# Performance work log

Hardware: AMD Instinct MI355X
Metric: run time of the kernel (lower is better)

## Reference

```python
import jax, jax.numpy as jnp
import numpy as np

B, T, D = 32, 200, 256
H, DH = 4, 32
INNER = H * DH  # 128
L, FF, NI = 8, 1024, 100000
NB = 64  # gap/recency buckets


def _ln(x, g, b, eps=1e-5):
    m = x.mean(-1, keepdims=True)
    v = jnp.mean((x - m) ** 2, -1, keepdims=True)
    return (x - m) / jnp.sqrt(v + eps) * g + b


def _gelu(x):
    return jax.nn.gelu(x, approximate=False)


def _dwconv_causal(x, w, b):
    # x: [B,T,C], w: [C,k] depthwise kernel, causal left-pad (k-1)
    k = w.shape[1]
    xp = jnp.pad(x, ((0, 0), (k - 1, 0), (0, 0))).transpose(0, 2, 1)  # [B,C,T+k-1]
    out = jax.lax.conv_general_dilated(
        xp, w[:, None, :], (1,), 'VALID',
        dimension_numbers=('NCH', 'OIH', 'NCH'), feature_group_count=w.shape[0])
    return out.transpose(0, 2, 1) + b


def _causal_linear_attention(q, k, v, m4):
    q = (jax.nn.elu(q) + 1.0) * m4
    k = (jax.nn.elu(k) + 1.0) * m4
    v = v * m4
    kv = jnp.einsum('bthd,bthe->bthde', k, v)          # [B,T,H,DH,DH]
    kv_prefix = jnp.cumsum(kv, axis=1)
    k_prefix = jnp.cumsum(k, axis=1)
    num = jnp.einsum('bthd,bthde->bthe', q, kv_prefix)
    den = jnp.sum(q * k_prefix, -1, keepdims=True)
    return num / (den + 1e-6) * m4


def _forward(item_emb, pos_emb, gap_emb, rec_emb, tf_w1, tf_b1, tf_w2, tf_b2,
             in_g, in_b, l_ln1g, l_ln1b, l_win, l_bin, l_wc, l_bc, l_tw, l_tb,
             l_pw, l_pb, l_wmix, l_bmix, l_ln2g, l_ln2b, l_wf1, l_bf1, l_wf2, l_bf2,
             fn_g, fn_b, pg_w, pg_b, uh_w1, uh_b1, uh_lng, uh_lnb, uh_w2, uh_b2,
             item_bias, ids, ts, lens):
    Bb, Tt = ids.shape
    pos = jnp.arange(Tt)
    mask = pos[None, :] >= (Tt - lens)[:, None]  # right-aligned valid mask [B,T]
    prev_ts = jnp.roll(ts, 1, axis=1)
    prev_mask = jnp.roll(mask, 1, axis=1).at[:, 0].set(False)
    zero = jnp.zeros_like(ts)
    gap_vals = jnp.where(mask & prev_mask, jnp.maximum(ts - prev_ts, 0), zero)
    latest = ts[:, -1:]
    rec_vals = jnp.where(mask, jnp.maximum(latest - ts, 0), zero)

    def buck(v, n):
        vf = jnp.maximum(v.astype(jnp.float32), 0.0)
        return jnp.clip(jnp.floor(jnp.log2(vf + 1.0)), 0, n - 1).astype(jnp.int32)

    gb = buck(gap_vals, NB)
    rb = buck(rec_vals, NB)
    rec_raw = jnp.maximum(latest - ts, 0).astype(jnp.float32)
    tf = jnp.stack([jnp.log1p(gb.astype(jnp.float32)), jnp.log1p(rec_raw)], -1)  # [B,T,2]
    dense_time = _gelu(tf @ tf_w1 + tf_b1) @ tf_w2 + tf_b2

    x = item_emb[ids] + pos_emb[None] + gap_emb[gb] + rec_emb[rb] + dense_time
    mf = mask[..., None].astype(x.dtype)
    m4 = mask[..., None, None].astype(x.dtype)
    x = _ln(x, in_g, in_b) * mf

    for i in range(L):
        res = x
        nrm = _ln(x, l_ln1g[i], l_ln1b[i])
        proj = nrm @ l_win[i] + l_bin[i]  # [B,T,D+3*INNER]
        gate = proj[..., :D]
        q = proj[..., D:D + INNER].reshape(Bb, Tt, H, DH)
        k = proj[..., D + INNER:D + 2 * INNER].reshape(Bb, Tt, H, DH)
        v = proj[..., D + 2 * INNER:].reshape(Bb, Tt, H, DH)
        content = _causal_linear_attention(q, k, v, m4).reshape(Bb, Tt, INNER) @ l_wc[i] + l_bc[i]
        temporal = _dwconv_causal(nrm, l_tw[i], l_tb[i])
        positional = _dwconv_causal(nrm, l_pw[i], l_pb[i])
        mixed = jnp.concatenate([content, temporal, positional], -1) @ l_wmix[i] + l_bmix[i]
        x = (res + jax.nn.sigmoid(gate) * mixed) * mf
        h = _ln(x, l_ln2g[i], l_ln2b[i])
        ffn = _gelu(h @ l_wf1[i] + l_bf1[i]) @ l_wf2[i] + l_bf2[i]
        x = (x + ffn) * mf

    x = _ln(x, fn_g, fn_b) * mf
    denom = jnp.maximum(lens, 1)[:, None].astype(x.dtype)
    mean_pooled = (x * mf).sum(1) / denom
    ps = (x @ pg_w + pg_b)[..., 0]
    ps = jnp.where(mask, ps, -1e9)
    pw = jax.nn.softmax(ps, axis=1)[..., None]
    attn_pooled = (pw * x).sum(1)
    last = x[:, -1, :]
    u = jnp.concatenate([last, mean_pooled, attn_pooled], -1)
    u = _gelu(u @ uh_w1 + uh_b1)
    u = _ln(u, uh_lng, uh_lnb)
    u = u @ uh_w2 + uh_b2
    u = u / jnp.maximum(jnp.linalg.norm(u, axis=-1, keepdims=True), 1e-12)
    ie = item_emb[1:]
    ie = ie / jnp.maximum(jnp.linalg.norm(ie, axis=-1, keepdims=True), 1e-12)
    return u @ ie.T + item_bias[1:]


def setup_inputs() -> dict:
    key = jax.random.key(0)
    it = iter(jax.random.split(key, 64))
    def nk():
        return next(it)
    def w(*s):
        return jax.random.normal(nk(), s, jnp.float32) * 0.02
    inp = dict(
        history_ids=jax.random.randint(nk(), (B, T), 0, NI),
        history_timestamps=jnp.sort(jax.random.randint(nk(), (B, T), 0, 1000000), axis=1),
        history_lengths=jax.random.randint(nk(), (B,), 1, T + 1),
        item_emb=w(NI + 1, D).at[0].set(0.0),
        pos_emb=w(T, D), gap_emb=w(NB, D), rec_emb=w(NB, D),
        tf_w1=w(2, D), tf_b1=jnp.zeros((D,)), tf_w2=w(D, D), tf_b2=jnp.zeros((D,)),
        in_g=jnp.ones((D,)), in_b=jnp.zeros((D,)),
        l_ln1g=jnp.ones((L, D)), l_ln1b=jnp.zeros((L, D)),
        l_win=w(L, D, D + 3 * INNER), l_bin=jnp.zeros((L, D + 3 * INNER)),
        l_wc=w(L, INNER, D), l_bc=jnp.zeros((L, D)),
        l_tw=w(L, D, 3), l_tb=jnp.zeros((L, D)),
        l_pw=w(L, D, 5), l_pb=jnp.zeros((L, D)),
        l_wmix=w(L, 3 * D, D), l_bmix=jnp.zeros((L, D)),
        l_ln2g=jnp.ones((L, D)), l_ln2b=jnp.zeros((L, D)),
        l_wf1=w(L, D, FF), l_bf1=jnp.zeros((L, FF)),
        l_wf2=w(L, FF, D), l_bf2=jnp.zeros((L, D)),
        fn_g=jnp.ones((D,)), fn_b=jnp.zeros((D,)),
        pg_w=w(D, 1), pg_b=jnp.zeros((1,)),
        uh_w1=w(3 * D, 1024), uh_b1=jnp.zeros((1024,)),
        uh_lng=jnp.ones((1024,)), uh_lnb=jnp.zeros((1024,)),
        uh_w2=w(1024, D), uh_b2=jnp.zeros((D,)),
        item_bias=jnp.zeros((NI + 1,)),
    )
    return inp


def reference(history_ids, history_timestamps, history_lengths, item_emb, pos_emb,
              gap_emb, rec_emb, tf_w1, tf_b1, tf_w2, tf_b2, in_g, in_b, l_ln1g,
              l_ln1b, l_win, l_bin, l_wc, l_bc, l_tw, l_tb, l_pw, l_pb, l_wmix,
              l_bmix, l_ln2g, l_ln2b, l_wf1, l_bf1, l_wf2, l_bf2, fn_g, fn_b,
              pg_w, pg_b, uh_w1, uh_b1, uh_lng, uh_lnb, uh_w2, uh_b2, item_bias):
    return _forward(item_emb, pos_emb, gap_emb, rec_emb, tf_w1, tf_b1, tf_w2, tf_b2,
                    in_g, in_b, l_ln1g, l_ln1b, l_win, l_bin, l_wc, l_bc, l_tw, l_tb,
                    l_pw, l_pb, l_wmix, l_bmix, l_ln2g, l_ln2b, l_wf1, l_bf1, l_wf2,
                    l_bf2, fn_g, fn_b, pg_w, pg_b, uh_w1, uh_b1, uh_lng, uh_lnb,
                    uh_w2, uh_b2, item_bias, history_ids, history_timestamps,
                    history_lengths)
```

## Files before the change

kernel.cpp:

```cpp
#include <hip/hip_runtime.h>
#include <math.h>

#define B_ 32
#define T_ 200
#define D_ 256
#define H_ 4
#define DH_ 32
#define INNER_ 128
#define L_ 8
#define FF_ 1024
#define NI_ 100000
#define NB_ 64
#define CH_ 25

typedef __attribute__((ext_vector_type(8))) short short8;
typedef __attribute__((ext_vector_type(8))) unsigned short ushort8;
typedef __attribute__((ext_vector_type(4))) unsigned short ushort4v;
typedef __attribute__((ext_vector_type(4))) float floatx4;

__device__ __forceinline__ float gelu_f(float x){
  return 0.5f*x*(1.0f+erff(x*0.70710678118654752f));
}
__device__ __forceinline__ float wsum(float v){
  #pragma unroll
// ... 155 lines not shown
      int m0 = bm + wm + 16*i + kg*4;
      #pragma unroll
      for (int r=0;r<4;r++){
        int m = m0 + r;
        if (m < M){
          float v = acc[i][j][r] + bv;
          if (mode == 1) v = gelu_f(v);
          float* cp = &C[(size_t)m*ldC + n];
          if (mode == 2) v += *cp;
          *cp = v;
        }
      }
    }
  }
}

template<int K, int NJ>
__global__ __launch_bounds__(256) void k_gemm16(
    const unsigned short* __restrict__ A, const unsigned short* __restrict__ Wt,
    const float* __restrict__ bias, void* __restrict__ Cv,
    int ldA, int ldW, int ldC, int mode)
{
  int tid = threadIdx.x;
  int wave = tid >> 6, lane = tid & 63;
  int frow = lane & 15, kg = lane >> 4;
  int bm = blockIdx.y * 32;
  int bn = blockIdx.x * (64*NJ) + wave * (16*NJ);

  const unsigned short* a0 = A + (size_t)(bm + frow)*ldA + kg*8;
  const unsigned short* a1 = a0 + (size_t)16*ldA;
  const unsigned short* b0 = Wt + (size_t)(bn + frow)*ldW + kg*8;

  floatx4 acc[2][NJ];
  #pragma unroll
  for (int i=0;i<2;i++)
    #pragma unroll
    for (int j=0;j<NJ;j++) acc[i][j] = (floatx4){0.f,0.f,0.f,0.f};

  #pragma unroll
  for (int k0=0; k0<K; k0+=32){
    short8 af0 = *(const short8*)(a0 + k0);
    short8 af1 = *(const short8*)(a1 + k0);
    #pragma unroll
    for (int j=0;j<NJ;j++){
      short8 bf = *(const short8*)(b0 + (size_t)j*16*ldW + k0);
      acc[0][j] = __builtin_amdgcn_mfma_f32_16x16x32_bf16(af0, bf, acc[0][j], 0, 0, 0);
      acc[1][j] = __builtin_amdgcn_mfma_f32_16x16x32_bf16(af1, bf, acc[1][j], 0, 0, 0);
    }
  }

  float* Cf = (float*)Cv;
  unsigned short* Ch = (unsigned short*)Cv;
  #pragma unroll
  for (int j=0;j<NJ;j++){
    int n = bn + 16*j + frow;
    float bv = bias[n];
    #pragma unroll
    for (int i=0;i<2;i++){
      int m0 = bm + 16*i + kg*4;
      #pragma unroll
      for (int r=0;r<4;r++){
        float v = acc[i][j][r] + bv;
        size_t off = (size_t)(m0+r)*ldC + n;
        if (mode == 1)      Cf[off] = gelu_f(v);
        else if (mode == 2) Cf[off] += v;
        else if (mode == 4) Ch[off] = f2bf(gelu_f(v));
        else                Cf[off] = v;
      }
    }
  }
}

__global__ __launch_bounds__(256) void k_proj(
  const unsigned short* __restrict__ A, const unsigned short* __restrict__ Wt,
  const float* __restrict__ bias, const int* __restrict__ lens,
  unsigned short* __restrict__ gateb, unsigned short* __restrict__ phiQ,
  unsigned short* __restrict__ phiK, unsigned short* __restrict__ vB,
  const float* __restrict__ tw, const float* __restrict__ tb,
  const float* __restrict__ pw, const float* __restrict__ pb,
  unsigned short* __restrict__ cat)
{
  int bid = blockIdx.x;
  int tid = threadIdx.x;
  if (bid < 400){
    int wave = tid >> 6, lane = tid & 63;
    int frow = lane & 15, kg = lane >> 4;
    int bx = bid & 1, by = bid >> 1;
    int bm = by * 32;
    int wn = bx*320 + wave*80;
    const unsigned short* a0 = A + (size_t)(bm + frow)*256 + kg*8;
    const unsigned short* a1 = a0 + (size_t)16*256;
    const unsigned short* b0 = Wt + (size_t)(wn + frow)*256 + kg*8;
    floatx4 acc[2][5];
    #pragma unroll
    for (int i=0;i<2;i++)
      #pragma unroll
      for (int j=0;j<5;j++) acc[i][j] = (floatx4){0.f,0.f,0.f,0.f};
    #pragma unroll
    for (int k0=0; k0<256; k0+=32){
      short8 af0 = *(const short8*)(a0 + k0);
      short8 af1 = *(const short8*)(a1 + k0);
      #pragma unroll
      for (int j=0;j<5;j++){
        short8 bf = *(const short8*)(b0 + (size_t)j*16*256 + k0);
        acc[0][j] = __builtin_amdgcn_mfma_f32_16x16x32_bf16(af0, bf, acc[0][j], 0, 0, 0);
        acc[1][j] = __builtin_amdgcn_mfma_f32_16x16x32_bf16(af1, bf, acc[1][j], 0, 0, 0);
      }
    }
    #pragma unroll
    for (int i=0;i<2;i++){
      #pragma unroll
      for (int r=0;r<4;r++){
        int row = bm + 16*i + kg*4 + r;
        int t = row % T_, b = row / T_;
        float m = (t >= T_ - lens[b]) ? 1.f : 0.f;
        #pragma unroll
        for (int j=0;j<5;j++){
          int n = wn + 16*j + frow;
          float v = acc[i][j][r] + bias[n];
          if (n < 256){
            gateb[(size_t)row*256 + n] = f2bf(v);
          } else if (n < 384){
            int bh = b*4 + ((n-256)>>5), dd = n & 31;
            phiQ[(size_t)bh*6400 + t*32 + dd] = f2bf((v > 0.f ? v + 1.f : __expf(v))*m);
          } else if (n < 512){
            int bh = b*4 + ((n-384)>>5), dd = n & 31;
            phiK[(size_t)bh*6400 + t*32 + dd] = f2bf((v > 0.f ? v + 1.f : __expf(v))*m);
          } else {
            int bh = b*4 + ((n-512)>>5), dd = n & 31;
            vB[(size_t)bh*6400 + t*32 + dd] = f2bf(v*m);
          }
        }
      }
    }
  } else {
    int bid2 = bid - 400;
    int d = tid;
    int bt0 = bid2*4;
    float xs8[8];
    #pragma unroll
    for (int w=0;w<8;w++){
      int wr = bt0 - 4 + w;
      xs8[w] = (wr >= 0) ? bf2f(A[(size_t)wr*256 + d]) : 0.f;
    }
    #pragma unroll
    for (int rr=0;rr<4;rr++){
      int bt = bt0 + rr, t = bt % T_;
      float ot = tb[d], op = pb[d];
      #pragma unroll
      for (int j=0;j<5;j++){
        int tt = t - 4 + j;
        float xv = (tt >= 0) ? xs8[rr+j] : 0.f;
        op += pw[d*5+j]*xv;
        if (j >= 2) ot += tw[d*3 + (j-2)]*xv;
      }
      cat[(size_t)bt*640 + 128 + d] = f2bf(ot);
      cat[(size_t)bt*640 + 384 + d] = f2bf(op);
    }
  }
}

template<int K, int MODE>
__global__ __launch_bounds__(256) void k_gemmln(
    const unsigned short* __restrict__ A, const unsigned short* __restrict__ Wt,
    const float* __restrict__ bias, float* __restrict__ xbuf,
    const unsigned short* __restrict__ gateb, const int* __restrict__ lens,
    const float* __restrict__ g, const float* __restrict__ bb,
    unsigned short* __restrict__ nrm, int maskLN)
{
  __shared__ float rs[16][4];
  __shared__ float rq[16][4];
  int tid = threadIdx.x;
  int wave = tid >> 6, lane = tid & 63;
  int frow = lane & 15, kg = lane >> 4;
  int bm = blockIdx.x * 16;
  int wn = wave * 64;

  const unsigned short* a0 = A + (size_t)(bm + frow)*K + kg*8;
  const unsigned short* b0 = Wt + (size_t)(wn + frow)*K + kg*8;

  floatx4 acc[4];
  #pragma unroll
  for (int j=0;j<4;j++) acc[j] = (floatx4){0.f,0.f,0.f,0.f};

  #pragma unroll
  for (int k0=0; k0<K; k0+=32){
    short8 af0 = *(const short8*)(a0 + k0);
    #pragma unroll
    for (int j=0;j<4;j++){
      short8 bf = *(const short8*)(b0 + (size_t)16*j*K + k0);
      acc[j] = __builtin_amdgcn_mfma_f32_16x16x32_bf16(af0, bf, acc[j], 0, 0, 0);
    }
  }

  float xn[4][4];
  float rowm[4];
  #pragma unroll
  for (int r=0;r<4;r++){
    int row = bm + kg*4 + r;
    int t = row % T_, b = row / T_;
    float m = (t >= T_ - lens[b]) ? 1.f : 0.f;
    rowm[r] = m;
    #pragma unroll
    for (int j=0;j<4;j++){
      int n = wn + 16*j + frow;
      float v = acc[j][r] + bias[n];
      float xv = xbuf[(size_t)row*256 + n];
      float xnv;
      if (MODE == 0){
        float gv = bf2f(gateb[(size_t)row*256 + n]);
        xnv = (xv + v/(1.f+__expf(-gv)))*m;
      } else {
        xnv = (xv + v)*m;
      }
      xn[j][r] = xnv;
      xbuf[(size_t)row*256 + n] = xnv;
    }
  }
  float mu[4];
  #pragma unroll
  for (int r=0;r<4;r++){
    float s = xn[0][r]+xn[1][r]+xn[2][r]+xn[3][r];
    s += __shfl_xor(s,1,64); s += __shfl_xor(s,2,64);
    s += __shfl_xor(s,4,64); s += __shfl_xor(s,8,64);
    if (frow == 0) rs[kg*4 + r][wave] = s;
  }
  __syncthreads();
  #pragma unroll
  for (int r=0;r<4;r++){
    int rl = kg*4 + r;
    mu[r] = (rs[rl][0]+rs[rl][1]+rs[rl][2]+rs[rl][3]) * (1.f/256.f);
  }
  float rstd[4];
  #pragma unroll
  for (int r=0;r<4;r++){
    float m0 = mu[r];
    float s = 0.f;
    #pragma unroll
    for (int j=0;j<4;j++){ float d = xn[j][r]-m0; s += d*d; }
    s += __shfl_xor(s,1,64); s += __shfl_xor(s,2,64);
    s += __shfl_xor(s,4,64); s += __shfl_xor(s,8,64);
    if (frow == 0) rq[kg*4 + r][wave] = s;
  }
  __syncthreads();
  #pragma unroll
  for (int r=0;r<4;r++){
    int rl = kg*4 + r;
    float q = rq[rl][0]+rq[rl][1]+rq[rl][2]+rq[rl][3];
    rstd[r] = rsqrtf(q*(1.f/256.f) + 1e-5f);
  }
  #pragma unroll
  for (int r=0;r<4;r++){
    int row = bm + kg*4 + r;
    float ml = maskLN ? rowm[r] : 1.f;
    #pragma unroll
    for (int j=0;j<4;j++){
      int n = wn + 16*j + frow;
      float h = (xn[j][r]-mu[r])*rstd[r]*g[n] + bb[n];
      nrm[(size_t)row*256 + n] = f2bf(h*ml);
    }
  }
}

__global__ __launch_bounds__(256) void k_embed(
  const int* __restrict__ ids, const int* __restrict__ ts, const int* __restrict__ lens,
  const float* __restrict__ item_emb, const float* __restrict__ pos_emb,
  const float* __restrict__ gap_emb, const float* __restrict__ rec_emb,
  const float* __restrict__ tf_w1, const float* __restrict__ tf_b1,
  float* __restrict__ xbuf, unsigned short* __restrict__ tfh)
{
  int bt = blockIdx.x;
  int b = bt / T_, t = bt % T_;
  int d = threadIdx.x;
  int len = lens[b];
  int tcur = ts[b*T_+t];
  int tlast = ts[b*T_+T_-1];
  bool mask  = t >= T_ - len;
  bool pmask = (t >= 1) && ((t-1) >= T_ - len);
  int gap = 0;
  if (mask && pmask){ int pv = ts[b*T_+t-1]; gap = max(tcur - pv, 0); }
  int rec = mask ? max(tlast - tcur, 0) : 0;
  int gb = min(max((int)floorf(log2f((float)gap + 1.0f)), 0), NB_-1);
  int rb = min(max((int)floorf(log2f((float)rec + 1.0f)), 0), NB_-1);
  float rec_raw = (float)max(tlast - tcur, 0);
  float tf0 = log1pf((float)gb);
  float tf1 = log1pf(rec_raw);
  float hid = gelu_f(tf0*tf_w1[d] + tf1*tf_w1[D_+d] + tf_b1[d]);
  tfh[(size_t)bt*D_ + d] = f2bf(hid);
  int id = ids[b*T_+t];
  xbuf[(size_t)bt*D_ + d] = item_emb[(size_t)id*D_ + d] + pos_emb[t*D_ + d]
                          + gap_emb[gb*D_ + d] + rec_emb[rb*D_ + d];
}

template<int NC>
__global__ __launch_bounds__(256) void k_ln(
  const float* __restrict__ in, void* __restrict__ out,
  const float* __restrict__ g, const float* __restrict__ bb,
  int rows, const int* __restrict__ lens, int applyMask, int outBf)
{
  int wid = threadIdx.x >> 6, lane = threadIdx.x & 63;
  int r = blockIdx.x*4 + wid;
  if (r >= rows) return;
  const int D = NC*256;
  const float4* rp = (const float4*)(in + (size_t)r*D);
  float4 v[NC];
  float s = 0.f;
  #pragma unroll
  for (int c=0;c<NC;c++){ v[c] = rp[c*64 + lane]; s += v[c].x+v[c].y+v[c].z+v[c].w; }
  s = wsum(s);
  float mean = s / (float)D;
  float q = 0.f;
  #pragma unroll
  for (int c=0;c<NC;c++){
    float a=v[c].x-mean, b2=v[c].y-mean, c2=v[c].z-mean, d2=v[c].w-mean;
    q += a*a + b2*b2 + c2*c2 + d2*d2;
  }
  q = wsum(q);
  float rstd = rsqrtf(q/(float)D + 1e-5f);
  float m = 1.f;
  if (applyMask){ int t = r % T_; int b = r / T_; m = (t >= T_ - lens[b]) ? 1.f : 0.f; }
  #pragma unroll
  for (int c=0;c<NC;c++){
    float4 gg  = ((const float4*)g )[c*64+lane];
    float4 bv  = ((const float4*)bb)[c*64+lane];
    float4 o;
    o.x = ((v[c].x-mean)*rstd*gg.x + bv.x)*m;
    o.y = ((v[c].y-mean)*rstd*gg.y + bv.y)*m;
    o.z = ((v[c].z-mean)*rstd*gg.z + bv.z)*m;
    o.w = ((v[c].w-mean)*rstd*gg.w + bv.w)*m;
    if (outBf){
      ushort4v ob; ob.x=f2bf(o.x); ob.y=f2bf(o.y); ob.z=f2bf(o.z); ob.w=f2bf(o.w);
      ((ushort4v*)((unsigned short*)out + (size_t)r*D))[c*64+lane] = ob;
    } else {
      ((float4*)((float*)out + (size_t)r*D))[c*64+lane] = o;
    }
  }
}

__global__ __launch_bounds__(256) void k_lnln(
  float* __restrict__ x, const int* __restrict__ lens,
  const float* __restrict__ g1, const float* __restrict__ b1,
  const float* __restrict__ g2, const float* __restrict__ b2,
  unsigned short* __restrict__ nrm)
{
  int wid = threadIdx.x >> 6, lane = threadIdx.x & 63;
  int r = blockIdx.x*4 + wid;
  int t = r % T_, b = r / T_;
  float m = (t >= T_ - lens[b]) ? 1.f : 0.f;
  float4 v = ((const float4*)(x + (size_t)r*256))[lane];
  float s = wsum(v.x+v.y+v.z+v.w);
  float mean = s/256.f;
  float a=v.x-mean, b2v=v.y-mean, c2=v.z-mean, d2=v.w-mean;
  float q = wsum(a*a+b2v*b2v+c2*c2+d2*d2);
  float rstd = rsqrtf(q/256.f + 1e-5f);
  float4 gg = ((const float4*)g1)[lane];
  float4 bv = ((const float4*)b1)[lane];
  float4 xn;
  xn.x = (a*rstd*gg.x + bv.x)*m;
  xn.y = (b2v*rstd*gg.y + bv.y)*m;
  xn.z = (c2*rstd*gg.z + bv.z)*m;
  xn.w = (d2*rstd*gg.w + bv.w)*m;
  ((float4*)(x + (size_t)r*256))[lane] = xn;
  float s2 = wsum(xn.x+xn.y+xn.z+xn.w);
  float mean2 = s2/256.f;
  float a2=xn.x-mean2, b22=xn.y-mean2, c22=xn.z-mean2, d22=xn.w-mean2;
  float q2 = wsum(a2*a2+b22*b22+c22*c22+d22*d22);
  float rstd2 = rsqrtf(q2/256.f + 1e-5f);
  float4 gg2 = ((const float4*)g2)[lane];
  float4 bv2 = ((const float4*)b2)[lane];
  ushort4v o;
  o.x = f2bf(a2*rstd2*gg2.x + bv2.x);
  o.y = f2bf(b22*rstd2*gg2.y + bv2.y);
  o.z = f2bf(c22*rstd2*gg2.z + bv2.z);
  o.w = f2bf(d22*rstd2*gg2.w + bv2.w);
  ((ushort4v*)(nrm + (size_t)r*256))[lane] = o;
}

__global__ __launch_bounds__(128) void k_attn_sums(
  const unsigned short* __restrict__ phiK, const unsigned short* __restrict__ vB,
  float* __restrict__ Ssum)
{
  int blk = blockIdx.x;
  int bh = blk >> 3, c = blk & 7;
  int tid = threadIdx.x; int e = tid & 31, q = tid >> 5;
  __shared__ float sk[CH_*32], sv[CH_*32];
  size_t base = (size_t)bh*6400 + (size_t)c*CH_*32;
  for (int idx = tid; idx < CH_*32; idx += 128){
    sk[idx] = bf2f(phiK[base + idx]);
    sv[idx] = bf2f(vB[base + idx]);
  }
  __syncthreads();
  float acc[8];
  #pragma unroll
  for (int j=0;j<8;j++) acc[j]=0.f;
  for (int tl=0; tl<CH_; tl++){
    const float4* k4 = (const float4*)(sk + tl*32 + q*8);
    float vf = sv[tl*32 + e];
    float4 ka = k4[0], kb = k4[1];
    acc[0]+=ka.x*vf; acc[1]+=ka.y*vf; acc[2]+=ka.z*vf; acc[3]+=ka.w*vf;
    acc[4]+=kb.x*vf; acc[5]+=kb.y*vf; acc[6]+=kb.z*vf; acc[7]+=kb.w*vf;
  }
  float* dst = Ssum + ((size_t)bh*8 + c)*1056;
  #pragma unroll
  for (int j=0;j<8;j++) dst[(q*8+j)*32 + e] = acc[j];
  if (q == 0){
    float s = 0.f;
    for (int tl=0; tl<CH_; tl++) s += sk[tl*32 + e];
    dst[1024 + e] = s;
  }
}

__global__ __launch_bounds__(256) void k_attn_out(
  const unsigned short* __restrict__ phiQ, const unsigned short* __restrict__ phiK,
  const unsigned short* __restrict__ vB, const int* __restrict__ lens,
  const float* __restrict__ Ssum, unsigned short* __restrict__ cat)
{
  int blk = blockIdx.x;
  int bh = blk >> 3, c = blk & 7;
  int b = bh >> 2, h = bh & 3;
  int tid = threadIdx.x; int e = tid & 31, qg = tid >> 5;
  int tstart = T_ - lens[b];
  __shared__ float sq[CH_*32], sk[CH_*32], sv[CH_*32];
  __shared__ float P[1056];
  __shared__ float A[CH_][CH_+1];
  __shared__ float sden[CH_];
  int t0 = c*CH_;
  const float* basep = Ssum + (size_t)bh*8*1056;
  for (int idx = tid; idx < 1056; idx += 256){
    float s = 0.f;
    for (int cp=0; cp<c; cp++) s += basep[(size_t)cp*1056 + idx];
    P[idx] = s;
  }
  size_t base = (size_t)bh*6400 + (size_t)c*CH_*32;
  for (int idx = tid; idx < CH_*32; idx += 256){
    sq[idx] = bf2f(phiQ[base + idx]);
    sk[idx] = bf2f(phiK[base + idx]);
    sv[idx] = bf2f(vB[base + idx]);
  }
  __syncthreads();
  for (int idx = tid; idx < CH_*CH_; idx += 256){
    int t = idx / CH_, tp = idx - t*CH_;
    float s = 0.f;
    if (tp <= t){
      const float4* q4 = (const float4*)(sq + t*32);
      const float4* k4 = (const float4*)(sk + tp*32);
      #pragma unroll
      for (int jj=0;jj<8;jj++){
        float4 qq = q4[jj], kk = k4[jj];
        s += qq.x*kk.x + qq.y*kk.y + qq.z*kk.z + qq.w*kk.w;
      }
    }
    A[t][tp] = s;
  }
  __syncthreads();
  if (tid < CH_){
    int t = tid;
    float s = 0.f;
    for (int tp=0; tp<=t; tp++) s += A[t][tp];
    const float* qf = sq + t*32;
    #pragma unroll
    for (int d=0; d<32; d++) s += qf[d]*P[1024+d];
    sden[t] = s;
  }
  __syncthreads();
  int tlo = (qg*CH_) >> 3, thi = ((qg+1)*CH_) >> 3;
  for (int t = tlo; t < thi; t++){
    float num = 0.f;
    for (int tp=0; tp<=t; tp++) num += A[t][tp]*sv[tp*32+e];
    const float* qf = sq + t*32;
    #pragma unroll
    for (int d=0; d<32; d++) num += qf[d]*P[d*32+e];
    int tg = t0 + t;
    float m = (tg >= tstart) ? 1.f : 0.f;
    cat[(size_t)(b*T_+tg)*640 + h*32 + e] = f2bf(num/(sden[t]+1e-6f)*m);
  }
}

__global__ __launch_bounds__(256) void k_pool(
  const unsigned short* __restrict__ x, const int* __restrict__ lens,
  const float* __restrict__ pg_w, const float* __restrict__ pg_b,
  float* __restrict__ u0)
{
  int b = blockIdx.x;
  int tid = threadIdx.x, wid = tid>>6, lane = tid&63;
  __shared__ float sps[T_];
  __shared__ float spw[T_];
  int len = lens[b]; int tstart = T_ - len;
  const float4* pw4 = (const float4*)pg_w;
  float4 wv = pw4[lane];
  for (int t = wid; t < T_; t += 4){
    ushort4v xv = ((const ushort4v*)(x + (size_t)(b*T_+t)*D_))[lane];
    float dot = bf2f(xv.x)*wv.x + bf2f(xv.y)*wv.y + bf2f(xv.z)*wv.z + bf2f(xv.w)*wv.w;
    dot = wsum(dot);
    if (lane==0) sps[t] = (t >= tstart) ? dot + pg_b[0] : -1e9f;
  }
  __syncthreads();
  float mx = -1e30f;
  for (int t=0;t<T_;t++) mx = fmaxf(mx, sps[t]);
  float sum = 0.f;
  for (int t=0;t<T_;t++) sum += __expf(sps[t]-mx);
  float inv = 1.f/sum;
  if (tid < T_) spw[tid] = __expf(sps[tid]-mx)*inv;
  __syncthreads();
  int d = tid;
  float macc=0.f, aacc=0.f;
  for (int t=0;t<T_;t++){
    float v = bf2f(x[(size_t)(b*T_+t)*D_ + d]);
    macc += v;
    aacc += spw[t]*v;
  }
  u0[b*768 + d]       = bf2f(x[(size_t)(b*T_+T_-1)*D_ + d]);
  u0[b*768 + 256 + d] = macc / (float)max(len,1);
  u0[b*768 + 512 + d] = aacc;
}

__global__ __launch_bounds__(64) void k_norm(float* __restrict__ u, unsigned short* __restrict__ ub)
{
  int b = blockIdx.x; int lane = threadIdx.x;
  float4* r = (float4*)(u + b*256);
  float4 v = r[lane];
  float ss = v.x*v.x + v.y*v.y + v.z*v.z + v.w*v.w;
  ss = wsum(ss);
  float sc = 1.f/fmaxf(sqrtf(ss), 1e-12f);
  v.x*=sc; v.y*=sc; v.z*=sc; v.w*=sc;
  r[lane]=v;
  ub[b*256 + lane*4 + 0] = f2bf(v.x);
  ub[b*256 + lane*4 + 1] = f2bf(v.y);
  ub[b*256 + lane*4 + 2] = f2bf(v.z);
  ub[b*256 + lane*4 + 3] = f2bf(v.w);
}

__global__ __launch_bounds__(256) void k_score2(
  const float* __restrict__ item_emb, const unsigned short* __restrict__ ub,
  const float* __restrict__ item_bias, float* __restrict__ out)
{
  int tid = threadIdx.x;
  int wave = tid >> 6, lane = tid & 63;
  int frow = lane & 15, kg = lane >> 4;
  int n0 = blockIdx.x * 128 + wave * 32;

  int g0 = n0 + frow, g1 = n0 + 16 + frow;
  bool ok0 = g0 < NI_, ok1 = g1 < NI_;
  const float* ip0 = item_emb + (size_t)(g0+1)*256 + kg*8;
  const float* ip1 = item_emb + (size_t)(g1+1)*256 + kg*8;
  const unsigned short* up0 = ub + frow*256 + kg*8;
  const unsigned short* up1 = up0 + 16*256;

  floatx4 acc[2][2];
  #pragma unroll
  for (int i=0;i<2;i++)
    #pragma unroll
    for (int j=0;j<2;j++) acc[i][j] = (floatx4){0.f,0.f,0.f,0.f};
  float ss0 = 0.f, ss1 = 0.f;

  #pragma unroll
  for (int k0=0; k0<256; k0+=32){
    float4 a0, a1, c0, c1;
    if (ok0){ a0 = *(const float4*)(ip0 + k0); a1 = *(const float4*)(ip0 + k0 + 4); }
// ... 34 lines not shown
    }
    #pragma unroll
    for (int j=0;j<2;j++){
      int row = 16*j + frow;
      float4 o;
      o.x = acc[i][j][0]*sc[0] + bv[0];
      o.y = acc[i][j][1]*sc[1] + bv[1];
      o.z = acc[i][j][2]*sc[2] + bv[2];
      o.w = acc[i][j][3]*sc[3] + bv[3];
      *(float4*)&out[(size_t)row*NI_ + nb] = o;
    }
  }
}

extern "C" void kernel_launch(void* const* d_in, const int* in_sizes, int n_in,
                              void* d_out, int out_size, void* d_ws, size_t ws_size,
                              hipStream_t stream)
{
  const int* ids  = (const int*)d_in[0];
  const int* ts   = (const int*)d_in[1];
  const int* lens = (const int*)d_in[2];
  const float* item_emb = (const float*)d_in[3];
  const float* pos_emb  = (const float*)d_in[4];
  const float* gap_emb  = (const float*)d_in[5];
  const float* rec_emb  = (const float*)d_in[6];
  const float* tf_w1 = (const float*)d_in[7];
  const float* tf_b1 = (const float*)d_in[8];
  const float* tf_w2 = (const float*)d_in[9];
  const float* tf_b2 = (const float*)d_in[10];
  const float* in_g  = (const float*)d_in[11];
  const float* in_b  = (const float*)d_in[12];
  const float* l_ln1g = (const float*)d_in[13];
  const float* l_ln1b = (const float*)d_in[14];
  const float* l_win  = (const float*)d_in[15];
  const float* l_bin  = (const float*)d_in[16];
  const float* l_wc   = (const float*)d_in[17];
  const float* l_bc   = (const float*)d_in[18];
  const float* l_tw   = (const float*)d_in[19];
  const float* l_tb   = (const float*)d_in[20];
  const float* l_pw   = (const float*)d_in[21];
  const float* l_pb   = (const float*)d_in[22];
  const float* l_wmix = (const float*)d_in[23];
  const float* l_bmix = (const float*)d_in[24];
  const float* l_ln2g = (const float*)d_in[25];
  const float* l_ln2b = (const float*)d_in[26];
  const float* l_wf1  = (const float*)d_in[27];
  const float* l_bf1  = (const float*)d_in[28];
  const float* l_wf2  = (const float*)d_in[29];
  const float* l_bf2  = (const float*)d_in[30];
  const float* fn_g = (const float*)d_in[31];
  const float* fn_b = (const float*)d_in[32];
  const float* pg_w = (const float*)d_in[33];
  const float* pg_b = (const float*)d_in[34];
  const float* uh_w1 = (const float*)d_in[35];
  const float* uh_b1 = (const float*)d_in[36];
  const float* uh_lng = (const float*)d_in[37];
  const float* uh_lnb = (const float*)d_in[38];
  const float* uh_w2 = (const float*)d_in[39];
  const float* uh_b2 = (const float*)d_in[40];
  const float* item_bias = (const float*)d_in[41];
  float* out = (float*)d_out;

  const int MT = B_*T_;
  float* ws   = (float*)d_ws;
  float* xbuf = ws;
  float* tmp  = xbuf + (size_t)MT*D_;
  float* proj = tmp  + (size_t)MT*D_;
  float* cat  = proj + (size_t)MT*640;
  float* mid  = cat  + (size_t)MT*640;
  float* u0   = mid  + (size_t)MT*FF_;
  float* u1   = u0 + 32*768;
  float* u2   = u1 + 32*1024;
  float* WcombF = u2 + 32*256;
  float* bmixP  = WcombF + 262144;
  float* Ssum   = bmixP + 2048;
  unsigned short* WtPerm = (unsigned short*)(Ssum + 1081344);
  unsigned short* WtMixT = WtPerm + 5505024;
  unsigned short* WtBig  = WtMixT + 1572864;
  unsigned short* WtH    = WtBig  + 1310720;
  unsigned short* u2b    = WtH    + 1114112;

  unsigned short* tmpb = (unsigned short*)tmp;
  unsigned short* catb = (unsigned short*)cat;
  unsigned short* midb = (unsigned short*)(mid + (size_t)MT*D_);
  unsigned short* gateb = (unsigned short*)proj;
  unsigned short* phiQ  = gateb + 1638400;
  unsigned short* phiK  = phiQ + 819200;
  unsigned short* vBuf  = phiK + 819200;

  k_cvtAll<<<8008, 256, 0, stream>>>(l_win, l_wmix, l_wf1, l_wf2, tf_w2, uh_w1, uh_w2,
                                     WtPerm, WtMixT, WtH, l_bc, l_bmix, bmixP);
  k_gemm_bf<64><<<dim3(4,1,8), 256, 0, stream>>>(l_wc, WtMixT, nullptr, WcombF,
                                                 128, 256, 256, 256, 768, 256, 0,
                                                 (size_t)128*256, (size_t)196608, (size_t)32768, 0);
  k_asm<<<64, 256, 0, stream>>>(WcombF, WtMixT, WtBig);

  k_embed<<<MT, 256, 0, stream>>>(ids, ts, lens, item_emb, pos_emb, gap_emb, rec_emb,
                                  tf_w1, tf_b1, xbuf, tmpb);
  k_gemm16<256,2><<<dim3(2,200), 256, 0, stream>>>(tmpb, WtH, tf_b2, xbuf, 256, 256, 256, 2);
  k_lnln<<<MT/4, 256, 0, stream>>>(xbuf, lens, in_g, in_b, l_ln1g, l_ln1b, tmpb);

  for (int i=0;i<L_;i++){
    const unsigned short* WL = WtPerm + (size_t)i*688128;
    k_proj<<<2000, 256, 0, stream>>>(tmpb, WL, l_bin+i*640, lens,
                                     gateb, phiQ, phiK, vBuf,
                                     l_tw+i*768, l_tb+i*256, l_pw+i*1280, l_pb+i*256, catb);
    k_attn_sums<<<B_*H_*8, 128, 0, stream>>>(phiK, vBuf, Ssum);
    k_attn_out<<<B_*H_*8, 256, 0, stream>>>(phiQ, phiK, vBuf, lens, Ssum, catb);
    k_gemmln<640,0><<<400, 256, 0, stream>>>(catb, WtBig+(size_t)i*163840, bmixP+i*256,
                                             xbuf, gateb, lens,
                                             l_ln2g+i*256, l_ln2b+i*256, tmpb, 0);
    k_gemm16<256,4><<<dim3(4,200), 256, 0, stream>>>(tmpb, WL+163840, l_bf1+i*FF_, midb,
                                                     256, 256, FF_, 4);
    bool last = (i == L_-1);
    k_gemmln<1024,1><<<400, 256, 0, stream>>>(midb, WL+425984, l_bf2+i*256,
                                              xbuf, nullptr, lens,
                                              last ? fn_g : l_ln1g+(i+1)*256,
                                              last ? fn_b : l_ln1b+(i+1)*256,
                                              tmpb, last ? 1 : 0);
  }

  k_pool<<<B_, 256, 0, stream>>>(tmpb, lens, pg_w, pg_b, u0);
  k_gemm_bf<128><<<dim3(8,1), 256, 0, stream>>>(u0, WtH+65536, uh_b1, u1,
                                                32, 1024, 768, 768, 768, 1024, 1, 0,0,0,0);
  k_ln<4><<<8, 256, 0, stream>>>(u1, u1, uh_lng, uh_lnb, 32, lens, 0, 0);
  k_gemm_bf<64><<<dim3(4,1), 256, 0, stream>>>(u1, WtH+851968, uh_b2, u2,
                                               32, 256, 1024, 1024, 1024, 256, 0, 0,0,0,0);
  k_norm<<<B_, 64, 0, stream>>>(u2, u2b);

  k_score2<<<(NI_+127)/128, 256, 0, stream>>>(item_emb, u2b, item_bias, out);
}
```

Before: 1.687 ms.

## Fuse attention passes and the mix+LN+FFN+LN chain into single kernels

Merges the two attention kernels into one that recomputes prefix KV sums from earlier chunks in shared memory instead of going through a global Ssum buffer. Fuses the mix GEMM, gated residual, LN2, both FFN GEMMs with GELU, residual and the next LN into one per-16-row kernel that keeps the hidden activations in LDS, removing the mid buffer round trip and two launches per layer. It also halves the k_proj row tile to double its block count. In exchange the attention does redundant prefix work for later chunks, and the fused MLP has only 400 blocks with heavy LDS use and reloads the FFN weights per block.

```diff
diff --git a/kernel.cpp b/kernel.cpp
--- a/kernel.cpp
+++ b/kernel.cpp
@@ -261,59 +261,51 @@
 {
   int bid = blockIdx.x;
   int tid = threadIdx.x;
-  if (bid < 400){
+  if (bid < 800){
     int wave = tid >> 6, lane = tid & 63;
     int frow = lane & 15, kg = lane >> 4;
     int bx = bid & 1, by = bid >> 1;
-    int bm = by * 32;
+    int bm = by * 16;
     int wn = bx*320 + wave*80;
     const unsigned short* a0 = A + (size_t)(bm + frow)*256 + kg*8;
-    const unsigned short* a1 = a0 + (size_t)16*256;
     const unsigned short* b0 = Wt + (size_t)(wn + frow)*256 + kg*8;
-    floatx4 acc[2][5];
-    #pragma unroll
-    for (int i=0;i<2;i++)
-      #pragma unroll
-      for (int j=0;j<5;j++) acc[i][j] = (floatx4){0.f,0.f,0.f,0.f};
+    floatx4 acc[5];
+    #pragma unroll
+    for (int j=0;j<5;j++) acc[j] = (floatx4){0.f,0.f,0.f,0.f};
     #pragma unroll
     for (int k0=0; k0<256; k0+=32){
       short8 af0 = *(const short8*)(a0 + k0);
-      short8 af1 = *(const short8*)(a1 + k0);
       #pragma unroll
       for (int j=0;j<5;j++){
         short8 bf = *(const short8*)(b0 + (size_t)j*16*256 + k0);
-        acc[0][j] = __builtin_amdgcn_mfma_f32_16x16x32_bf16(af0, bf, acc[0][j], 0, 0, 0);
-        acc[1][j] = __builtin_amdgcn_mfma_f32_16x16x32_bf16(af1, bf, acc[1][j], 0, 0, 0);
+        acc[j] = __builtin_amdgcn_mfma_f32_16x16x32_bf16(af0, bf, acc[j], 0, 0, 0);
       }
     }
     #pragma unroll
-    for (int i=0;i<2;i++){
+    for (int r=0;r<4;r++){
+      int row = bm + kg*4 + r;
+      int t = row % T_, b = row / T_;
+      float m = (t >= T_ - lens[b]) ? 1.f : 0.f;
       #pragma unroll
-      for (int r=0;r<4;r++){
-        int row = bm + 16*i + kg*4 + r;
-        int t = row % T_, b = row / T_;
-        float m = (t >= T_ - lens[b]) ? 1.f : 0.f;
-        #pragma unroll
-        for (int j=0;j<5;j++){
-          int n = wn + 16*j + frow;
-          float v = acc[i][j][r] + bias[n];
-          if (n < 256){
-            gateb[(size_t)row*256 + n] = f2bf(v);
-          } else if (n < 384){
-            int bh = b*4 + ((n-256)>>5), dd = n & 31;
-            phiQ[(size_t)bh*6400 + t*32 + dd] = f2bf((v > 0.f ? v + 1.f : __expf(v))*m);
-          } else if (n < 512){
-            int bh = b*4 + ((n-384)>>5), dd = n & 31;
-            phiK[(size_t)bh*6400 + t*32 + dd] = f2bf((v > 0.f ? v + 1.f : __expf(v))*m);
-          } else {
-            int bh = b*4 + ((n-512)>>5), dd = n & 31;
-            vB[(size_t)bh*6400 + t*32 + dd] = f2bf(v*m);
-          }
+      for (int j=0;j<5;j++){
+        int n = wn + 16*j + frow;
+        float v = acc[j][r] + bias[n];
+        if (n < 256){
+          gateb[(size_t)row*256 + n] = f2bf(v);
+        } else if (n < 384){
+          int bh = b*4 + ((n-256)>>5), dd = n & 31;
+          phiQ[(size_t)bh*6400 + t*32 + dd] = f2bf((v > 0.f ? v + 1.f : __expf(v))*m);
+        } else if (n < 512){
+          int bh = b*4 + ((n-384)>>5), dd = n & 31;
+          phiK[(size_t)bh*6400 + t*32 + dd] = f2bf((v > 0.f ? v + 1.f : __expf(v))*m);
+        } else {
+          int bh = b*4 + ((n-512)>>5), dd = n & 31;
+          vB[(size_t)bh*6400 + t*32 + dd] = f2bf(v*m);
         }
       }
     }
   } else {
-    int bid2 = bid - 400;
+    int bid2 = bid - 800;
     int d = tid;
     int bt0 = bid2*4;
     float xs8[8];
@@ -339,14 +331,106 @@
   }
 }
 
-template<int K, int MODE>
-__global__ __launch_bounds__(256) void k_gemmln(
-    const unsigned short* __restrict__ A, const unsigned short* __restrict__ Wt,
-    const float* __restrict__ bias, float* __restrict__ xbuf,
-    const unsigned short* __restrict__ gateb, const int* __restrict__ lens,
-    const float* __restrict__ g, const float* __restrict__ bb,
-    unsigned short* __restrict__ nrm, int maskLN)
-{
+__global__ __launch_bounds__(256) void k_attn_fused(
+  const unsigned short* __restrict__ phiQ, const unsigned short* __restrict__ phiK,
+  const unsigned short* __restrict__ vB, const int* __restrict__ lens,
+  unsigned short* __restrict__ cat)
+{
+  int blk = blockIdx.x;
+  int bh = blk >> 3, c = blk & 7;
+  int b = bh >> 2, h = bh & 3;
+  int tid = threadIdx.x; int e = tid & 31, qg = tid >> 5;
+  int tstart = T_ - lens[b];
+  __shared__ float sq[CH_*32], sk[CH_*32], sv[CH_*32];
+  __shared__ float P[1056];
+  __shared__ float A[CH_][CH_+1];
+  __shared__ float sden[CH_];
+  int t0 = c*CH_;
+  size_t bbase = (size_t)bh*6400;
+  float pkv0=0.f, pkv1=0.f, pkv2=0.f, pkv3=0.f, pks=0.f;
+  int dd = tid >> 3;
+  int e0 = (tid*4) & 31;
+  for (int cp=0; cp<c; cp++){
+    size_t pbase = bbase + (size_t)cp*800;
+    for (int idx=tid; idx<800; idx+=256){
+      sk[idx] = bf2f(phiK[pbase+idx]);
+      sv[idx] = bf2f(vB[pbase+idx]);
+    }
+    __syncthreads();
+    #pragma unroll 5
+    for (int tl=0; tl<CH_; tl++){
+      float kd = sk[tl*32+dd];
+      pkv0 += kd*sv[tl*32+e0];
+      pkv1 += kd*sv[tl*32+e0+1];
+      pkv2 += kd*sv[tl*32+e0+2];
+      pkv3 += kd*sv[tl*32+e0+3];
+    }
+    if (tid < 32){
+      float s = 0.f;
+      for (int tl=0; tl<CH_; tl++) s += sk[tl*32+tid];
+      pks += s;
+    }
+    __syncthreads();
+  }
+  P[tid*4+0]=pkv0; P[tid*4+1]=pkv1; P[tid*4+2]=pkv2; P[tid*4+3]=pkv3;
+  if (tid < 32) P[1024+tid] = pks;
+  size_t base = bbase + (size_t)c*800;
+  for (int idx=tid; idx<800; idx+=256){
+    sq[idx] = bf2f(phiQ[base+idx]);
+    sk[idx] = bf2f(phiK[base+idx]);
+    sv[idx] = bf2f(vB[base+idx]);
+  }
+  __syncthreads();
+  for (int idx = tid; idx < CH_*CH_; idx += 256){
+    int t = idx / CH_, tp = idx - t*CH_;
+    float s = 0.f;
+    if (tp <= t){
+      const float4* q4 = (const float4*)(sq + t*32);
+      const float4* k4 = (const float4*)(sk + tp*32);
+      #pragma unroll
+      for (int jj=0;jj<8;jj++){
+        float4 qq = q4[jj], kk = k4[jj];
+        s += qq.x*kk.x + qq.y*kk.y + qq.z*kk.z + qq.w*kk.w;
+      }
+    }
+    A[t][tp] = s;
+  }
+  __syncthreads();
+  if (tid < CH_){
+    int t = tid;
+    float s = 0.f;
+    for (int tp=0; tp<=t; tp++) s += A[t][tp];
+    const float* qf = sq + t*32;
+    #pragma unroll
+    for (int d=0; d<32; d++) s += qf[d]*P[1024+d];
+    sden[t] = s;
+  }
+  __syncthreads();
+  int tlo = (qg*CH_) >> 3, thi = ((qg+1)*CH_) >> 3;
+  for (int t = tlo; t < thi; t++){
+    float num = 0.f;
+    for (int tp=0; tp<=t; tp++) num += A[t][tp]*sv[tp*32+e];
+    const float* qf = sq + t*32;
+    #pragma unroll
+    for (int d=0; d<32; d++) num += qf[d]*P[d*32+e];
+    int tg = t0 + t;
+    float m = (tg >= tstart) ? 1.f : 0.f;
+    cat[(size_t)(b*T_+tg)*640 + h*32 + e] = f2bf(num/(sden[t]+1e-6f)*m);
+  }
+}
+
+__global__ __launch_bounds__(256) void k_mlp(
+  const unsigned short* __restrict__ catA, const unsigned short* __restrict__ Wmix,
+  const float* __restrict__ bmix, float* __restrict__ xbuf,
+  const unsigned short* __restrict__ gateb, const int* __restrict__ lens,
+  const float* __restrict__ g2, const float* __restrict__ b2,
+  const unsigned short* __restrict__ W1t, const float* __restrict__ bf1,
+  const unsigned short* __restrict__ W2t, const float* __restrict__ bf2,
+  const float* __restrict__ gn, const float* __restrict__ bn2,
+  unsigned short* __restrict__ nrm, int maskLN)
+{
+  __shared__ unsigned short hb[16][264];
+  __shared__ unsigned short ms[16][1032];
   __shared__ float rs[16][4];
   __shared__ float rq[16][4];
   int tid = threadIdx.x;
@@ -355,24 +439,21 @@
   int bm = blockIdx.x * 16;
   int wn = wave * 64;
 
-  const unsigned short* a0 = A + (size_t)(bm + frow)*K + kg*8;
-  const unsigned short* b0 = Wt + (size_t)(wn + frow)*K + kg*8;
-
+  const unsigned short* a0 = catA + (size_t)(bm + frow)*640 + kg*8;
+  const unsigned short* b0 = Wmix + (size_t)(wn + frow)*640 + kg*8;
   floatx4 acc[4];
   #pragma unroll
   for (int j=0;j<4;j++) acc[j] = (floatx4){0.f,0.f,0.f,0.f};
-
-  #pragma unroll
-  for (int k0=0; k0<K; k0+=32){
-    short8 af0 = *(const short8*)(a0 + k0);
+  #pragma unroll
+  for (int k0=0; k0<640; k0+=32){
+    short8 af = *(const short8*)(a0 + k0);
     #pragma unroll
     for (int j=0;j<4;j++){
-      short8 bf = *(const short8*)(b0 + (size_t)16*j*K + k0);
-      acc[j] = __builtin_amdgcn_mfma_f32_16x16x32_bf16(af0, bf, acc[j], 0, 0, 0);
-    }
-  }
-
-  float xn[4][4];
+      short8 bf = *(const short8*)(b0 + (size_t)j*16*640 + k0);
+      acc[j] = __builtin_amdgcn_mfma_f32_16x16x32_bf16(af, bf, acc[j], 0, 0, 0);
+    }
+  }
+  float xm[4][4];
   float rowm[4];
   #pragma unroll
   for (int r=0;r<4;r++){
@@ -383,23 +464,16 @@
     #pragma unroll
     for (int j=0;j<4;j++){
       int n = wn + 16*j + frow;
-      float v = acc[j][r] + bias[n];
+      float v = acc[j][r] + bmix[n];
       float xv = xbuf[(size_t)row*256 + n];
-      float xnv;
-      if (MODE == 0){
-        float gv = bf2f(gateb[(size_t)row*256 + n]);
-        xnv = (xv + v/(1.f+__expf(-gv)))*m;
-      } else {
-        xnv = (xv + v)*m;
-      }
-      xn[j][r] = xnv;
-      xbuf[(size_t)row*256 + n] = xnv;
-    }
-  }
-  float mu[4];
-  #pragma unroll
-  for (int r=0;r<4;r++){
-    float s = xn[0][r]+xn[1][r]+xn[2][r]+xn[3][r];
+      float gv = bf2f(gateb[(size_t)row*256 + n]);
+      xm[j][r] = (xv + v/(1.f+__expf(-gv)))*m;
+    }
+  }
+  float mu[4], rstd[4];
+  #pragma unroll
+  for (int r=0;r<4;r++){
+    float s = xm[0][r]+xm[1][r]+xm[2][r]+xm[3][r];
     s += __shfl_xor(s,1,64); s += __shfl_xor(s,2,64);
     s += __shfl_xor(s,4,64); s += __shfl_xor(s,8,64);
     if (frow == 0) rs[kg*4 + r][wave] = s;
@@ -410,13 +484,12 @@
     int rl = kg*4 + r;
     mu[r] = (rs[rl][0]+rs[rl][1]+rs[rl][2]+rs[rl][3]) * (1.f/256.f);
   }
-  float rstd[4];
   #pragma unroll
   for (int r=0;r<4;r++){
     float m0 = mu[r];
     float s = 0.f;
     #pragma unroll
-    for (int j=0;j<4;j++){ float d = xn[j][r]-m0; s += d*d; }
+    for (int j=0;j<4;j++){ float d = xm[j][r]-m0; s += d*d; }
     s += __shfl_xor(s,1,64); s += __shfl_xor(s,2,64);
     s += __shfl_xor(s,4,64); s += __shfl_xor(s,8,64);
     if (frow == 0) rq[kg*4 + r][wave] = s;
@@ -430,13 +503,106 @@
   }
   #pragma unroll
   for (int r=0;r<4;r++){
+    #pragma unroll
+    for (int j=0;j<4;j++){
+      int n = wn + 16*j + frow;
+      float hh = (xm[j][r]-mu[r])*rstd[r]*g2[n] + b2[n];
+      hb[kg*4+r][n] = f2bf(hh);
+    }
+  }
+  __syncthreads();
+
+  #pragma unroll 2
+  for (int jo=0; jo<8; jo++){
+    int nA = wave*256 + jo*32 + frow;
+    int nB = nA + 16;
+    const unsigned short* bpA = W1t + (size_t)nA*256 + kg*8;
+    const unsigned short* bpB = W1t + (size_t)nB*256 + kg*8;
+    floatx4 fA = (floatx4){0.f,0.f,0.f,0.f};
+    floatx4 fB = (floatx4){0.f,0.f,0.f,0.f};
+    #pragma unroll
+    for (int k0=0; k0<256; k0+=32){
+      short8 af = *(const short8*)&hb[frow][kg*8 + k0];
+      short8 b1v = *(const short8*)(bpA + k0);
+      short8 b2v = *(const short8*)(bpB + k0);
+      fA = __builtin_amdgcn_mfma_f32_16x16x32_bf16(af, b1v, fA, 0, 0, 0);
+      fB = __builtin_amdgcn_mfma_f32_16x16x32_bf16(af, b2v, fB, 0, 0, 0);
+    }
+    float bbA = bf1[nA], bbB = bf1[nB];
+    #pragma unroll
+    for (int r=0;r<4;r++){
+      ms[kg*4+r][nA] = f2bf(gelu_f(fA[r] + bbA));
+      ms[kg*4+r][nB] = f2bf(gelu_f(fB[r] + bbB));
+    }
+  }
+  __syncthreads();
+
+  floatx4 f2[4];
+  #pragma unroll
+  for (int j=0;j<4;j++) f2[j] = (floatx4){0.f,0.f,0.f,0.f};
+  const unsigned short* c0 = W2t + (size_t)(wn + frow)*1024 + kg*8;
+  #pragma unroll
+  for (int k0=0; k0<1024; k0+=32){
+    short8 af = *(const short8*)&ms[frow][kg*8 + k0];
+    #pragma unroll
+    for (int j=0;j<4;j++){
+      short8 bf = *(const short8*)(c0 + (size_t)j*16*1024 + k0);
+      f2[j] = __builtin_amdgcn_mfma_f32_16x16x32_bf16(af, bf, f2[j], 0, 0, 0);
+    }
+  }
+  float xn2[4][4];
+  #pragma unroll
+  for (int r=0;r<4;r++){
+    int row = bm + kg*4 + r;
+    #pragma unroll
+    for (int j=0;j<4;j++){
+      int n = wn + 16*j + frow;
+      float v = f2[j][r] + bf2[n];
+      float xnv = (xm[j][r] + v)*rowm[r];
+      xn2[j][r] = xnv;
+      xbuf[(size_t)row*256 + n] = xnv;
+    }
+  }
+  float mu2[4], rstd2[4];
+  #pragma unroll
+  for (int r=0;r<4;r++){
+    float s = xn2[0][r]+xn2[1][r]+xn2[2][r]+xn2[3][r];
+    s += __shfl_xor(s,1,64); s += __shfl_xor(s,2,64);
+    s += __shfl_xor(s,4,64); s += __shfl_xor(s,8,64);
+    if (frow == 0) rs[kg*4 + r][wave] = s;
+  }
+  __syncthreads();
+  #pragma unroll
+  for (int r=0;r<4;r++){
+    int rl = kg*4 + r;
+    mu2[r] = (rs[rl][0]+rs[rl][1]+rs[rl][2]+rs[rl][3]) * (1.f/256.f);
+  }
+  #pragma unroll
+  for (int r=0;r<4;r++){
+    float m0 = mu2[r];
+    float s = 0.f;
+    #pragma unroll
+    for (int j=0;j<4;j++){ float d = xn2[j][r]-m0; s += d*d; }
+    s += __shfl_xor(s,1,64); s += __shfl_xor(s,2,64);
+    s += __shfl_xor(s,4,64); s += __shfl_xor(s,8,64);
+    if (frow == 0) rq[kg*4 + r][wave] = s;
+  }
+  __syncthreads();
+  #pragma unroll
+  for (int r=0;r<4;r++){
+    int rl = kg*4 + r;
+    float q = rq[rl][0]+rq[rl][1]+rq[rl][2]+rq[rl][3];
+    rstd2[r] = rsqrtf(q*(1.f/256.f) + 1e-5f);
+  }
+  #pragma unroll
+  for (int r=0;r<4;r++){
     int row = bm + kg*4 + r;
     float ml = maskLN ? rowm[r] : 1.f;
     #pragma unroll
     for (int j=0;j<4;j++){
       int n = wn + 16*j + frow;
-      float h = (xn[j][r]-mu[r])*rstd[r]*g[n] + bb[n];
-      nrm[(size_t)row*256 + n] = f2bf(h*ml);
+      float hh = (xn2[j][r]-mu2[r])*rstd2[r]*gn[n] + bn2[n];
+      nrm[(size_t)row*256 + n] = f2bf(hh*ml);
     }
   }
 }
@@ -553,106 +719,6 @@
   o.z = f2bf(c22*rstd2*gg2.z + bv2.z);
   o.w = f2bf(d22*rstd2*gg2.w + bv2.w);
   ((ushort4v*)(nrm + (size_t)r*256))[lane] = o;
-}
-
-__global__ __launch_bounds__(128) void k_attn_sums(
-  const unsigned short* __restrict__ phiK, const unsigned short* __restrict__ vB,
-  float* __restrict__ Ssum)
-{
-  int blk = blockIdx.x;
-  int bh = blk >> 3, c = blk & 7;
-  int tid = threadIdx.x; int e = tid & 31, q = tid >> 5;
-  __shared__ float sk[CH_*32], sv[CH_*32];
-  size_t base = (size_t)bh*6400 + (size_t)c*CH_*32;
-  for (int idx = tid; idx < CH_*32; idx += 128){
-    sk[idx] = bf2f(phiK[base + idx]);
-    sv[idx] = bf2f(vB[base + idx]);
-  }
-  __syncthreads();
-  float acc[8];
-  #pragma unroll
-  for (int j=0;j<8;j++) acc[j]=0.f;
-  for (int tl=0; tl<CH_; tl++){
-    const float4* k4 = (const float4*)(sk + tl*32 + q*8);
-    float vf = sv[tl*32 + e];
-    float4 ka = k4[0], kb = k4[1];
-    acc[0]+=ka.x*vf; acc[1]+=ka.y*vf; acc[2]+=ka.z*vf; acc[3]+=ka.w*vf;
-    acc[4]+=kb.x*vf; acc[5]+=kb.y*vf; acc[6]+=kb.z*vf; acc[7]+=kb.w*vf;
-  }
-  float* dst = Ssum + ((size_t)bh*8 + c)*1056;
-  #pragma unroll
-  for (int j=0;j<8;j++) dst[(q*8+j)*32 + e] = acc[j];
-  if (q == 0){
-    float s = 0.f;
-    for (int tl=0; tl<CH_; tl++) s += sk[tl*32 + e];
-    dst[1024 + e] = s;
-  }
-}
-
-__global__ __launch_bounds__(256) void k_attn_out(
-  const unsigned short* __restrict__ phiQ, const unsigned short* __restrict__ phiK,
-  const unsigned short* __restrict__ vB, const int* __restrict__ lens,
-  const float* __restrict__ Ssum, unsigned short* __restrict__ cat)
-{
-  int blk = blockIdx.x;
-  int bh = blk >> 3, c = blk & 7;
-  int b = bh >> 2, h = bh & 3;
-  int tid = threadIdx.x; int e = tid & 31, qg = tid >> 5;
-  int tstart = T_ - lens[b];
-  __shared__ float sq[CH_*32], sk[CH_*32], sv[CH_*32];
-  __shared__ float P[1056];
-  __shared__ float A[CH_][CH_+1];
-  __shared__ float sden[CH_];
-  int t0 = c*CH_;
-  const float* basep = Ssum + (size_t)bh*8*1056;
-  for (int idx = tid; idx < 1056; idx += 256){
-    float s = 0.f;
-    for (int cp=0; cp<c; cp++) s += basep[(size_t)cp*1056 + idx];
-    P[idx] = s;
-  }
-  size_t base = (size_t)bh*6400 + (size_t)c*CH_*32;
-  for (int idx = tid; idx < CH_*32; idx += 256){
-    sq[idx] = bf2f(phiQ[base + idx]);
-    sk[idx] = bf2f(phiK[base + idx]);
-    sv[idx] = bf2f(vB[base + idx]);
-  }
-  __syncthreads();
-  for (int idx = tid; idx < CH_*CH_; idx += 256){
-    int t = idx / CH_, tp = idx - t*CH_;
-    float s = 0.f;
-    if (tp <= t){
-      const float4* q4 = (const float4*)(sq + t*32);
-      const float4* k4 = (const float4*)(sk + tp*32);
-      #pragma unroll
-      for (int jj=0;jj<8;jj++){
-        float4 qq = q4[jj], kk = k4[jj];
-        s += qq.x*kk.x + qq.y*kk.y + qq.z*kk.z + qq.w*kk.w;
-      }
-    }
-    A[t][tp] = s;
-  }
-  __syncthreads();
-  if (tid < CH_){
-    int t = tid;
-    float s = 0.f;
-    for (int tp=0; tp<=t; tp++) s += A[t][tp];
-    const float* qf = sq + t*32;
-    #pragma unroll
-    for (int d=0; d<32; d++) s += qf[d]*P[1024+d];
-    sden[t] = s;
-  }
-  __syncthreads();
-  int tlo = (qg*CH_) >> 3, thi = ((qg+1)*CH_) >> 3;
-  for (int t = tlo; t < thi; t++){
-    float num = 0.f;
-    for (int tp=0; tp<=t; tp++) num += A[t][tp]*sv[tp*32+e];
-    const float* qf = sq + t*32;
-    #pragma unroll
-    for (int d=0; d<32; d++) num += qf[d]*P[d*32+e];
-    int tg = t0 + t;
-    float m = (tg >= tstart) ? 1.f : 0.f;
-    cat[(size_t)(b*T_+tg)*640 + h*32 + e] = f2bf(num/(sden[t]+1e-6f)*m);
-  }
 }
 
 __global__ __launch_bounds__(256) void k_pool(
@@ -853,7 +919,6 @@
 
   unsigned short* tmpb = (unsigned short*)tmp;
   unsigned short* catb = (unsigned short*)cat;
-  unsigned short* midb = (unsigned short*)(mid + (size_t)MT*D_);
   unsigned short* gateb = (unsigned short*)proj;
   unsigned short* phiQ  = gateb + 1638400;
   unsigned short* phiK  = phiQ + 819200;
@@ -873,22 +938,19 @@
 
   for (int i=0;i<L_;i++){
     const unsigned short* WL = WtPerm + (size_t)i*688128;
-    k_proj<<<2000, 256, 0, stream>>>(tmpb, WL, l_bin+i*640, lens,
+    bool last = (i == L_-1);
+    k_proj<<<2400, 256, 0, stream>>>(tmpb, WL, l_bin+i*640, lens,
                                      gateb, phiQ, phiK, vBuf,
                                      l_tw+i*768, l_tb+i*256, l_pw+i*1280, l_pb+i*256, catb);
-    k_attn_sums<<<B_*H_*8, 128, 0, stream>>>(phiK, vBuf, Ssum);
-    k_attn_out<<<B_*H_*8, 256, 0, stream>>>(phiQ, phiK, vBuf, lens, Ssum, catb);
-    k_gemmln<640,0><<<400, 256, 0, stream>>>(catb, WtBig+(size_t)i*163840, bmixP+i*256,
-                                             xbuf, gateb, lens,
-                                             l_ln2g+i*256, l_ln2b+i*256, tmpb, 0);
-    k_gemm16<256,4><<<dim3(4,200), 256, 0, stream>>>(tmpb, WL+163840, l_bf1+i*FF_, midb,
-                                                     256, 256, FF_, 4);
-    bool last = (i == L_-1);
-    k_gemmln<1024,1><<<400, 256, 0, stream>>>(midb, WL+425984, l_bf2+i*256,
-                                              xbuf, nullptr, lens,
-                                              last ? fn_g : l_ln1g+(i+1)*256,
-                                              last ? fn_b : l_ln1b+(i+1)*256,
-                                              tmpb, last ? 1 : 0);
+    k_attn_fused<<<B_*H_*8, 256, 0, stream>>>(phiQ, phiK, vBuf, lens, catb);
+    k_mlp<<<400, 256, 0, stream>>>(catb, WtBig+(size_t)i*163840, bmixP+i*256,
+                                   xbuf, gateb, lens,
+                                   l_ln2g+i*256, l_ln2b+i*256,
+                                   WL+163840, l_bf1+i*FF_,
+                                   WL+425984, l_bf2+i*256,
+                                   last ? fn_g : l_ln1g+(i+1)*256,
+                                   last ? fn_b : l_ln1b+(i+1)*256,
+                                   tmpb, last ? 1 : 0);
   }
 
   k_pool<<<B_, 256, 0, stream>>>(tmpb, lens, pg_w, pg_b, u0);
```

After: 1.602 ms. 1.05x faster.
